# Kernel tuning notes

Measured on AMD Instinct MI355X. Metric: run time of the kernel, lower is better.

Reference implementation:

```python
import jax, jax.numpy as jnp
import numpy as np
from jax import lax

B, N, S, K = 16, 4096, 1024, 32
RADIUS = 0.2
C_IN = 64
BN_EPS = 1e-5


def setup_inputs() -> dict:
    key = jax.random.key(0)
    ks = jax.random.split(key, 6)
    x = jax.random.normal(ks[0], (B, N, 3), dtype=jnp.float32)
    x_complete = jax.random.normal(ks[1], (B, N, C_IN), dtype=jnp.float32)
    W0 = jax.random.normal(ks[2], (64, 67), dtype=jnp.float32) * 0.1
    W1 = jax.random.normal(ks[3], (64, 64), dtype=jnp.float32) * 0.1
    W2 = jax.random.normal(ks[4], (128, 64), dtype=jnp.float32) * 0.1
    return {
        "x": x, "x_complete": x_complete,
        "W0": W0, "b0": jnp.zeros(64), "g0": jnp.ones(64), "be0": jnp.zeros(64),
        "W1": W1, "b1": jnp.zeros(64), "g1": jnp.ones(64), "be1": jnp.zeros(64),
        "W2": W2, "b2": jnp.zeros(128), "g2": jnp.ones(128), "be2": jnp.zeros(128),
    }


def _fps(xyz, n_samples):
    """Farthest point sampling. xyz: [B,N,3] -> indices [B,n_samples] (int32)."""
    b, n, _ = xyz.shape
    batch_ar = jnp.arange(b)

    def step(carry, _):
        dists, farthest = carry                      # [B,N], [B]
        centroid = xyz[batch_ar, farthest]           # [B,3]
        d = jnp.sum((xyz - centroid[:, None, :]) ** 2, axis=-1)  # [B,N]
        dists = jnp.minimum(dists, d)
        nxt = jnp.argmax(dists, axis=-1).astype(jnp.int32)
        return (dists, nxt), farthest

    init = (jnp.full((b, n), 1e10, dtype=xyz.dtype), jnp.zeros(b, dtype=jnp.int32))
    _, idx = lax.scan(step, init, None, length=n_samples)
    return idx.T                                     # [B,n_samples]


def _ball_query(xyz, new_xyz, radius, k):
    """First-k points within radius of each centroid. Returns [B,S,K] int32."""
    b, n, _ = xyz.shape
    # squared distances centroid->point: [B,S,N]
    d2 = jnp.sum((new_xyz[:, :, None, :] - xyz[:, None, :, :]) ** 2, axis=-1)
    idx = jnp.where(d2 <= radius * radius, jnp.arange(n, dtype=jnp.int32), jnp.int32(n))
    idx = jnp.sort(idx, axis=-1)[..., :k]            # first k in index order
    first = idx[..., :1]                             # centroid itself is always in ball
    idx = jnp.where(idx == n, first, idx)
    return jnp.minimum(idx, n - 1)


def _gather_points(pts, idx_flat):
    """pts [B,N,C], idx_flat [B,M] -> [B,M,C]."""
    return jnp.take_along_axis(pts, idx_flat[..., None], axis=1)


def _conv_bn_relu(f, W, b, g, be):
    """f [B,C,M]; 1x1 Conv1d + training-mode BatchNorm1d + ReLU."""
    y = jnp.einsum('bcm,dc->bdm', f, W) + b[None, :, None]
    mu = jnp.mean(y, axis=(0, 2), keepdims=True)
    var = jnp.var(y, axis=(0, 2), keepdims=True)
    y = (y - mu) * lax.rsqrt(var + BN_EPS) * g[None, :, None] + be[None, :, None]
    return jax.nn.relu(y)


def reference(x, x_complete, W0, b0, g0, be0, W1, b1, g1, be1, W2, b2, g2, be2):
    # 1) FPS sampling of S centroids
    fps_idx = _fps(x, S)                                     # [B,S]
    new_xyz = _gather_points(x, fps_idx)                     # [B,S,3]
    # 2) Ball-query grouping of K neighbors per centroid
    idx = _ball_query(x, new_xyz, RADIUS, K)                 # [B,S,K]
    idx_flat = idx.reshape(B, S * K)
    grouped_xyz = _gather_points(x, idx_flat).reshape(B, S, K, 3)
    grouped_xyz = grouped_xyz - new_xyz[:, :, None, :]       # relative coords
    grouped_feat = _gather_points(x_complete, idx_flat).reshape(B, S, K, C_IN)
    f = jnp.concatenate([grouped_xyz, grouped_feat], axis=-1)  # [B,S,K,67]
    # 3) Shared MLP over channel dim (Conv1d k=1 + BN + ReLU), channels-first
    f = f.reshape(B, S * K, 3 + C_IN).transpose(0, 2, 1)     # [B,67,S*K]
    f = _conv_bn_relu(f, W0, b0, g0, be0)
    f = _conv_bn_relu(f, W1, b1, g1, be1)
    f = _conv_bn_relu(f, W2, b2, g2, be2)                    # [B,128,S*K]
    # 4) Max-pool over the K neighbors per centroid
    out = jnp.max(f.reshape(B, 128, S, K), axis=3)           # [B,128,S]
    return out
```

## Files before the change

kernel.cpp:

```cpp
#include <hip/hip_runtime.h>

namespace {
constexpr int kB = 16;
constexpr int kN = 4096;
constexpr int kS = 1024;
constexpr int kK = 32;
constexpr int kCIN = 64;
constexpr int kCF = 67;
constexpr int kFD = 68;
constexpr int kSK = kS * kK;
constexpr int kPT = kB * kSK;
constexpr float kM = 524288.0f;

constexpr size_t kOffIdx   = 196608;
constexpr size_t kOffStats = 2293760;
constexpr size_t kOffScsh  = 2295808;
constexpr size_t kOffU     = 2297856;
constexpr size_t kWsNeedU  = kOffU + (size_t)kB * kN * 64 * sizeof(float);

constexpr int kLdsK = 72;

using bf16x8 = __attribute__((ext_vector_type(8))) short;
using f32x4  = __attribute__((ext_vector_type(4))) float;
}

__device__ __forceinline__ unsigned short f2bf(float f) {
  unsigned u = __float_as_uint(f);
  u += 0x7fffu + ((u >> 16) & 1u);
  return (unsigned short)(u >> 16);
}
__device__ __forceinline__ unsigned pack2bf(float a, float b) {
  return (unsigned)f2bf(a) | ((unsigned)f2bf(b) << 16);
}

__device__ void fps_body(const float* __restrict__ x, float* __restrict__ new_xyz,
                         int b, int tid, char* smem) {
  float* xs = (float*)smem;
  float* ys = xs + kN;
  float* zs = ys + kN;
  float* pv = zs + kN;
  int*   pi = (int*)(pv + 8);
  const int lane = tid & 63;
  const int wid = tid >> 6;
  const float* xb = x + (size_t)b * kN * 3;
  for (int q = tid; q < kN; q += 256) {
    xs[q] = xb[q * 3 + 0];
    ys[q] = xb[q * 3 + 1];
    zs[q] = xb[q * 3 + 2];
  }
  __syncthreads();
  float px[16], py[16], pz[16], dm[16];
#pragma unroll
  for (int j = 0; j < 16; ++j) {
    const int p = tid * 16 + j;
    px[j] = xs[p]; py[j] = ys[p]; pz[j] = zs[p];
    dm[j] = 1e10f;
  }
  int far = 0;
  for (int i = 0; i < kS; ++i) {
    const float cx = xs[far], cy = ys[far], cz = zs[far];
    if (tid == 0) {
      float* o = new_xyz + ((size_t)b * kS + i) * 3;
      o[0] = cx; o[1] = cy; o[2] = cz;
    }
#pragma unroll
    for (int j = 0; j < 16; ++j) {
      const float dx = __fsub_rn(px[j], cx);
      const float dy = __fsub_rn(py[j], cy);
      const float dz = __fsub_rn(pz[j], cz);
      const float t = __fadd_rn(__fadd_rn(__fmul_rn(dx, dx), __fmul_rn(dy, dy)),
                                __fmul_rn(dz, dz));
      dm[j] = fminf(dm[j], t);
    }
    float t8[8], t4[4], t2[2];
#pragma unroll
    for (int j = 0; j < 8; ++j) t8[j] = fmaxf(dm[j], dm[j + 8]);
#pragma unroll
    for (int j = 0; j < 4; ++j) t4[j] = fmaxf(t8[j], t8[j + 4]);
#pragma unroll
    for (int j = 0; j < 2; ++j) t2[j] = fmaxf(t4[j], t4[j + 2]);
    const float bv = fmaxf(t2[0], t2[1]);
    float wv = bv;
#pragma unroll
    for (int k = 1; k < 64; k <<= 1) wv = fmaxf(wv, __shfl_xor(wv, k, 64));
    unsigned msk = 0;
#pragma unroll
    for (int j = 0; j < 16; ++j) msk |= (dm[j] == bv ? 1u : 0u) << j;
    const unsigned long long bal = __ballot(bv == wv);
    const int win = (int)__builtin_ctzll(bal);
    const unsigned wmsk = (unsigned)__shfl((int)msk, win, 64);
    const int wfar = (wid * 64 + win) * 16 + (int)__builtin_ctz(wmsk);
    const int par = i & 1;
    if (lane == 0) { pv[par * 4 + wid] = wv; pi[par * 4 + wid] = wfar; }
    __syncthreads();
    float fv = pv[par * 4 + 0];
    int fi = pi[par * 4 + 0];
#pragma unroll
    for (int w = 1; w < 4; ++w) {
      const float v2 = pv[par * 4 + w];
      const int i2 = pi[par * 4 + w];
      if (v2 > fv) { fv = v2; fi = i2; }
    }
    far = fi;
  }
}

__device__ void u_body(const float* __restrict__ xc, const float* __restrict__ W0,
                       float* __restrict__ U, int ublk, int tid, char* smem) {
  unsigned short* a_lds = (unsigned short*)smem;
  unsigned short* w_lds = (unsigned short*)(smem + 128 * kLdsK * 2);
  const int r0 = ublk * 128;
  {
    const int pt = tid >> 1, half = tid & 1;
    const float4* src = (const float4*)(xc + ((size_t)(r0 + pt)) * 64 + half * 32);
    unsigned* dst = (unsigned*)(a_lds + pt * kLdsK + half * 32);
#pragma unroll
    for (int i = 0; i < 8; ++i) {
      const float4 v = src[i];
      dst[2 * i + 0] = pack2bf(v.x, v.y);
      dst[2 * i + 1] = pack2bf(v.z, v.w);
    }
  }
  for (int e = tid; e < 64 * 64; e += 256) {
    const int d = e >> 6, k2 = e & 63;
    w_lds[d * kLdsK + k2] = f2bf(W0[d * kCF + 3 + k2]);
  }
  __syncthreads();
  const int w = tid >> 6, lane = tid & 63, lr = lane & 15, lk = lane >> 4;
  f32x4 acc[2][4];
#pragma unroll
  for (int mi = 0; mi < 2; ++mi)
#pragma unroll
    for (int ni = 0; ni < 4; ++ni) acc[mi][ni] = (f32x4){0.f, 0.f, 0.f, 0.f};
#pragma unroll
  for (int ks = 0; ks < 2; ++ks) {
    const int k = lk * 8 + ks * 32;
    const bf16x8 a0 = *(const bf16x8*)(a_lds + (32 * w + lr) * kLdsK + k);
    const bf16x8 a1 = *(const bf16x8*)(a_lds + (32 * w + 16 + lr) * kLdsK + k);
#pragma unroll
    for (int ni = 0; ni < 4; ++ni) {
      const bf16x8 bv = *(const bf16x8*)(w_lds + (16 * ni + lr) * kLdsK + k);
      acc[0][ni] = __builtin_amdgcn_mfma_f32_16x16x32_bf16(a0, bv, acc[0][ni], 0, 0, 0);
      acc[1][ni] = __builtin_amdgcn_mfma_f32_16x16x32_bf16(a1, bv, acc[1][ni], 0, 0, 0);
    }
  }
#pragma unroll
  for (int mi = 0; mi < 2; ++mi)
#pragma unroll
    for (int ni = 0; ni < 4; ++ni)
#pragma unroll
      for (int r = 0; r < 4; ++r) {
        const int row = 32 * w + 16 * mi + lk * 4 + r;
        U[((size_t)(r0 + row)) * 64 + 16 * ni + lr] = acc[mi][ni][r];
      }
}

__global__ __launch_bounds__(256) void k1_kernel(const float* __restrict__ x,
                                                 const float* __restrict__ xc,
                                                 const float* __restrict__ W0,
                                                 float* __restrict__ nxyz,
                                                 float* __restrict__ U) {
  __shared__ __align__(16) char smem[49664];
  if (blockIdx.x < 16) fps_body(x, nxyz, blockIdx.x, threadIdx.x, smem);
  else u_body(xc, W0, U, blockIdx.x - 16, threadIdx.x, smem);
}

__global__ __launch_bounds__(256) void ballq_kernel(const float* __restrict__ x,
                                                    const float* __restrict__ new_xyz,
                                                    int* __restrict__ idx) {
  const int g = blockIdx.x * 4 + (threadIdx.x >> 6);
  const int lane = threadIdx.x & 63;
  const int b = g >> 10;
  const float* xb = x + (size_t)b * kN * 3;
  const float nx = new_xyz[g * 3 + 0];
  const float ny = new_xyz[g * 3 + 1];
  const float nz = new_xyz[g * 3 + 2];
  const float RR = (float)(0.2 * 0.2);
  int cnt = 0;
  int first = -1;
  for (int c = 0; c < kN / 64 && cnt < kK; ++c) {
    const int p = c * 64 + lane;
    const float dx = __fsub_rn(xb[p * 3 + 0], nx);
    const float dy = __fsub_rn(xb[p * 3 + 1], ny);
    const float dz = __fsub_rn(xb[p * 3 + 2], nz);
    const float t = __fadd_rn(__fadd_rn(__fmul_rn(dx, dx), __fmul_rn(dy, dy)),
                              __fmul_rn(dz, dz));
    const bool within = (t <= RR);
    const unsigned long long m = __ballot(within);
    if (first < 0 && m != 0ull) first = c * 64 + __builtin_ctzll(m);
    const int pos = cnt + (int)__popcll(m & ((1ull << lane) - 1ull));
    if (within && pos < kK) idx[(size_t)g * kK + pos] = p;
    cnt += (int)__popcll(m);
  }
  for (int k2 = cnt + lane; k2 < kK; k2 += 64) idx[(size_t)g * kK + k2] = first;
}

__global__ __launch_bounds__(256) void stats0_kernel(
    const float* __restrict__ x, const float* __restrict__ nxyz,
    const int* __restrict__ idx, const float* __restrict__ U,
    const float* __restrict__ W0, const float* __restrict__ b0,
    float* __restrict__ stats) {
  __shared__ float4 w0c[64];
  __shared__ float red[128];
  const int tid = threadIdx.x;
  if (tid < 64) w0c[tid] = make_float4(W0[tid * kCF + 0], W0[tid * kCF + 1],
                                       W0[tid * kCF + 2], b0[tid]);
  if (tid < 128) red[tid] = 0.0f;
  __syncthreads();
  const int gid = blockIdx.x * 256 + tid;
  const int half = gid & 1;
  const int pbase = gid >> 1;
  float s[32], q[32];
#pragma unroll
  for (int i = 0; i < 32; ++i) { s[i] = 0.f; q[i] = 0.f; }
  for (int r = 0; r < 8; ++r) {
    const int pt = pbase + r * 65536;
    const int v = idx[pt];
    const int b = pt >> 15;
    const int sc = (pt & (kSK - 1)) >> 5;
    const float* xp = x + ((size_t)b * kN + v) * 3;
    const float* np = nxyz + ((size_t)b * kS + sc) * 3;
    const float rx = xp[0] - np[0], ry = xp[1] - np[1], rz = xp[2] - np[2];
    const float4* up = (const float4*)(U + ((size_t)b * kN + v) * 64 + half * 32);
#pragma unroll
    for (int i = 0; i < 8; ++i) {
      const float4 u4 = up[i];
      const float uu[4] = {u4.x, u4.y, u4.z, u4.w};
#pragma unroll
      for (int j = 0; j < 4; ++j) {
        const float4 wc = w0c[half * 32 + i * 4 + j];
        const float y = uu[j] + rx * wc.x + ry * wc.y + rz * wc.z + wc.w;
        s[i * 4 + j] += y;
        q[i * 4 + j] += y * y;
      }
    }
  }
#pragma unroll
  for (int i = 0; i < 32; ++i) {
    const int c = half * 32 + i;
    atomicAdd(&red[c], s[i]);
    atomicAdd(&red[64 + c], q[i]);
  }
  __syncthreads();
  if (tid < 128) atomicAdd(&stats[tid], red[tid]);
}

template <int STAGE>
__global__ __launch_bounds__(256) void mlp_kernel(
    const float* __restrict__ x, const float* __restrict__ nxyz,
    const int* __restrict__ idx, const float* __restrict__ U,
    const float* __restrict__ W0, const float* __restrict__ b0,
    const float* __restrict__ W1, const float* __restrict__ b1v,
    const float* __restrict__ W2, const float* __restrict__ b2v,
    const float* __restrict__ scsh, float* __restrict__ stats,
    float* __restrict__ out) {
  __shared__ unsigned short a_lds[128 * kLdsK];
  __shared__ unsigned short w_lds[128 * kLdsK];
  __shared__ float red[256];
  __shared__ float4 w0c[64];
  __shared__ float2 sc0l[64];
  const int tid = threadIdx.x;
  const int p0 = blockIdx.x * 128;
  red[tid] = 0.0f;
  if (tid < 64) {
    w0c[tid] = make_float4(W0[tid * kCF + 0], W0[tid * kCF + 1],
                           W0[tid * kCF + 2], b0[tid]);
    sc0l[tid] = make_float2(scsh[tid], scsh[64 + tid]);
  }
  for (int f = tid; f < 64 * 16; f += 256) {
    const int d = f >> 4, k4 = (f & 15) * 4;
    const float4 vw = *(const float4*)(W1 + d * 64 + k4);
    unsigned* dst = (unsigned*)(w_lds + d * kLdsK + k4);
    dst[0] = pack2bf(vw.x, vw.y);
    dst[1] = pack2bf(vw.z, vw.w);
  }
  __syncthreads();

  {
    const int pt = tid >> 1, half = tid & 1;
    const int pg = p0 + pt;
    const int v = idx[pg];
    const int b = pg >> 15;
    const int sct = (pg & (kSK - 1)) >> 5;
    const float* xp = x + ((size_t)b * kN + v) * 3;
    const float* np = nxyz + ((size_t)b * kS + sct) * 3;
    const float rx = xp[0] - np[0], ry = xp[1] - np[1], rz = xp[2] - np[2];
    const float4* up = (const float4*)(U + ((size_t)b * kN + v) * 64 + half * 32);
    unsigned* dst = (unsigned*)(a_lds + pt * kLdsK + half * 32);
#pragma unroll
    for (int i = 0; i < 8; ++i) {
      const float4 u4 = up[i];
      const float uu[4] = {u4.x, u4.y, u4.z, u4.w};
      float a1[4];
#pragma unroll
      for (int j = 0; j < 4; ++j) {
        const int c = half * 32 + i * 4 + j;
        const float4 wc = w0c[c];
        const float y = uu[j] + rx * wc.x + ry * wc.y + rz * wc.z + wc.w;
        const float2 ss = sc0l[c];
        a1[j] = fmaxf(fmaf(y, ss.x, ss.y), 0.0f);
      }
      dst[2 * i + 0] = pack2bf(a1[0], a1[1]);
      dst[2 * i + 1] = pack2bf(a1[2], a1[3]);
    }
  }
  __syncthreads();

  const int w = tid >> 6, lane = tid & 63, lr = lane & 15, lk = lane >> 4;

  f32x4 acc1[2][4];
#pragma unroll
  for (int mi = 0; mi < 2; ++mi)
#pragma unroll
    for (int ni = 0; ni < 4; ++ni) acc1[mi][ni] = (f32x4){0.f, 0.f, 0.f, 0.f};
#pragma unroll
  for (int ks = 0; ks < 2; ++ks) {
    const int k = lk * 8 + ks * 32;
    const bf16x8 a0 = *(const bf16x8*)(a_lds + (32 * w + lr) * kLdsK + k);
    const bf16x8 a1 = *(const bf16x8*)(a_lds + (32 * w + 16 + lr) * kLdsK + k);
#pragma unroll
    for (int ni = 0; ni < 4; ++ni) {
      const bf16x8 bv = *(const bf16x8*)(w_lds + (16 * ni + lr) * kLdsK + k);
      acc1[0][ni] = __builtin_amdgcn_mfma_f32_16x16x32_bf16(a0, bv, acc1[0][ni], 0, 0, 0);
      acc1[1][ni] = __builtin_amdgcn_mfma_f32_16x16x32_bf16(a1, bv, acc1[1][ni], 0, 0, 0);
    }
  }

  if constexpr (STAGE == 1) {
#pragma unroll
    for (int ni = 0; ni < 4; ++ni) {
      const int ch = 16 * ni + lr;
      const float bb = b1v[ch];
      float ss = 0.f, qq = 0.f;
#pragma unroll
      for (int mi = 0; mi < 2; ++mi)
#pragma unroll
        for (int r = 0; r < 4; ++r) {
          const float y = acc1[mi][ni][r] + bb;
          ss += y;
          qq += y * y;
        }
      atomicAdd(&red[ch], ss);
      atomicAdd(&red[64 + ch], qq);
    }
    __syncthreads();
    if (tid < 128) atomicAdd(&stats[128 + tid], red[tid]);
    return;
  } else {
    __syncthreads();
#pragma unroll
    for (int ni = 0; ni < 4; ++ni) {
      const int ch = 16 * ni + lr;
      const float bb = b1v[ch];
      const float sc1 = scsh[128 + ch], sh1 = scsh[192 + ch];
#pragma unroll
      for (int mi = 0; mi < 2; ++mi)
#pragma unroll
        for (int r = 0; r < 4; ++r) {
          const int row = 32 * w + 16 * mi + lk * 4 + r;
          const float val = fmaxf(fmaf(acc1[mi][ni][r] + bb, sc1, sh1), 0.0f);
          a_lds[row * kLdsK + ch] = f2bf(val);
        }
    }
    for (int f = tid; f < 128 * 16; f += 256) {
      const int d = f >> 4, k4 = (f & 15) * 4;
      const float4 vw = *(const float4*)(W2 + d * 64 + k4);
      unsigned* dst = (unsigned*)(w_lds + d * kLdsK + k4);
      dst[0] = pack2bf(vw.x, vw.y);
      dst[1] = pack2bf(vw.z, vw.w);
    }
    __syncthreads();

    f32x4 acc2[2][8];
#pragma unroll
    for (int mi = 0; mi < 2; ++mi)
#pragma unroll
      for (int ni = 0; ni < 8; ++ni) acc2[mi][ni] = (f32x4){0.f, 0.f, 0.f, 0.f};
#pragma unroll
    for (int ks = 0; ks < 2; ++ks) {
      const int k = lk * 8 + ks * 32;
      const bf16x8 a0 = *(const bf16x8*)(a_lds + (32 * w + lr) * kLdsK + k);
      const bf16x8 a1 = *(const bf16x8*)(a_lds + (32 * w + 16 + lr) * kLdsK + k);
#pragma unroll
      for (int ni = 0; ni < 8; ++ni) {
        const bf16x8 bv = *(const bf16x8*)(w_lds + (16 * ni + lr) * kLdsK + k);
        acc2[0][ni] = __builtin_amdgcn_mfma_f32_16x16x32_bf16(a0, bv, acc2[0][ni], 0, 0, 0);
        acc2[1][ni] = __builtin_amdgcn_mfma_f32_16x16x32_bf16(a1, bv, acc2[1][ni], 0, 0, 0);
      }
    }

    if constexpr (STAGE == 2) {
#pragma unroll
      for (int ni = 0; ni < 8; ++ni) {
        const int ch = 16 * ni + lr;
        const float bb = b2v[ch];
        float ss = 0.f, qq = 0.f;
#pragma unroll
        for (int mi = 0; mi < 2; ++mi)
#pragma unroll
          for (int r = 0; r < 4; ++r) {
            const float y = acc2[mi][ni][r] + bb;
            ss += y;
            qq += y * y;
          }
        atomicAdd(&red[ch], ss);
        atomicAdd(&red[128 + ch], qq);
      }
      __syncthreads();
      atomicAdd(&stats[256 + tid], red[tid]);
    } else {
      float mx[8];
#pragma unroll
      for (int ni = 0; ni < 8; ++ni) {
        const int ch = 16 * ni + lr;
        const float bb = b2v[ch];
        const float sc2 = scsh[256 + ch], sh2 = scsh[384 + ch];
        float m = -1.0f;
#pragma unroll
        for (int mi = 0; mi < 2; ++mi)
#pragma unroll
          for (int r = 0; r < 4; ++r)
            m = fmaxf(m, fmaxf(fmaf(acc2[mi][ni][r] + bb, sc2, sh2), 0.0f));
        mx[ni] = m;
      }
#pragma unroll
      for (int ni = 0; ni < 8; ++ni) {
        mx[ni] = fmaxf(mx[ni], __shfl_xor(mx[ni], 16, 64));
        mx[ni] = fmaxf(mx[ni], __shfl_xor(mx[ni], 32, 64));
      }
      const int pg0 = p0 + 32 * w;
      const int ob = pg0 >> 15;
      const int os = (pg0 & (kSK - 1)) >> 5;
      if (lane < 16) {
#pragma unroll
        for (int ni = 0; ni < 8; ++ni)
          out[((size_t)ob * 128 + 16 * ni + lane) * kS + os] = mx[ni];
      }
    }
  }
}

__global__ void finalize_kernel(const float* __restrict__ g, const float* __restrict__ be,
                                const float* __restrict__ st, float* __restrict__ sc,
                                float* __restrict__ sh, int C) {
  const int c = threadIdx.x;
  if (c < C) {
    const float mean = st[c] / kM;
    const float var = st[C + c] / kM - mean * mean;
    const float scale = g[c] / sqrtf(var + 1e-5f);
    sc[c] = scale;
    sh[c] = be[c] - mean * scale;
  }
}

__device__ __forceinline__ void load_bias4(float acc[4][4], const float* b, int tc) {
  const float4 bv = *(const float4*)(b + tc * 4);
  const float bb[4] = {bv.x, bv.y, bv.z, bv.w};
#pragma unroll
  for (int p2 = 0; p2 < 4; ++p2)
#pragma unroll
    for (int ci = 0; ci < 4; ++ci) acc[p2][ci] = bb[ci];
}

__device__ __forceinline__ void gemm4x4(const float* f_lds, const float* w_lds,
                                        int J, int tr, int tc, float acc[4][4]) {
  for (int j = 0; j < J; ++j) {
    const float4 w = *(const float4*)(w_lds + j * 64 + tc * 4);
#pragma unroll
    for (int p2 = 0; p2 < 4; ++p2) {
      const float fv = f_lds[(tr * 4 + p2) * kFD + j];
      acc[p2][0] = fmaf(fv, w.x, acc[p2][0]);
      acc[p2][1] = fmaf(fv, w.y, acc[p2][1]);
      acc[p2][2] = fmaf(fv, w.z, acc[p2][2]);
      acc[p2][3] = fmaf(fv, w.w, acc[p2][3]);
    }
  }
}

__device__ __forceinline__ void bnrelu4(float acc[4][4], const float* scp,
                                        const float* shp, int tc) {
  const float4 s4 = *(const float4*)(scp + tc * 4);
  const float4 h4 = *(const float4*)(shp + tc * 4);
  const float sv[4] = {s4.x, s4.y, s4.z, s4.w};
  const float hv[4] = {h4.x, h4.y, h4.z, h4.w};
#pragma unroll
  for (int p2 = 0; p2 < 4; ++p2)
#pragma unroll
    for (int ci = 0; ci < 4; ++ci)
      acc[p2][ci] = fmaxf(fmaf(acc[p2][ci], sv[ci], hv[ci]), 0.0f);
}

__device__ __forceinline__ void store_a4(const float acc[4][4], float* f_lds,
                                         int tr, int tc) {
#pragma unroll
  for (int p2 = 0; p2 < 4; ++p2)
#pragma unroll
    for (int ci = 0; ci < 4; ++ci)
      f_lds[(tr * 4 + p2) * kFD + tc * 4 + ci] = acc[p2][ci];
}

__device__ __forceinline__ void block_stats4(const float acc[4][4], float* red,
                                             int tc, int C) {
#pragma unroll
  for (int ci = 0; ci < 4; ++ci) {
    const int c = tc * 4 + ci;
    const float sv = acc[0][ci] + acc[1][ci] + acc[2][ci] + acc[3][ci];
    const float qv = acc[0][ci] * acc[0][ci] + acc[1][ci] * acc[1][ci] +
                     acc[2][ci] * acc[2][ci] + acc[3][ci] * acc[3][ci];
    atomicAdd(&red[c], sv);
    atomicAdd(&red[C + c], qv);
  }
}

__device__ __forceinline__ void gather_f(const float* __restrict__ x,
                                         const float* __restrict__ xc,
                                         const float* __restrict__ nxyz,
                                         const int* __restrict__ idx,
                                         float* f_lds, int p0, int tid) {
  const int th_p = tid >> 2;
  const int th_i = tid & 3;
  const int pg = p0 + th_p;
  const int b = pg >> 15;
  const int r = pg & (kSK - 1);
  const int s = r >> 5;
  const int v = idx[pg];
  const float4* feat = (const float4*)(xc + ((size_t)b * kN + v) * kCIN) + th_i * 4;
  const float4 q0 = feat[0], q1 = feat[1], q2 = feat[2], q3 = feat[3];
  float* dst = f_lds + th_p * kFD + 3 + th_i * 16;
  dst[0] = q0.x; dst[1] = q0.y; dst[2] = q0.z; dst[3] = q0.w;
  dst[4] = q1.x; dst[5] = q1.y; dst[6] = q1.z; dst[7] = q1.w;
  dst[8] = q2.x; dst[9] = q2.y; dst[10] = q2.z; dst[11] = q2.w;
  dst[12] = q3.x; dst[13] = q3.y; dst[14] = q3.z; dst[15] = q3.w;
  if (th_i == 0) {
    const float* xp = x + ((size_t)b * kN + v) * 3;
    const float* np = nxyz + ((size_t)b * kS + s) * 3;
    float* fr = f_lds + th_p * kFD;
    fr[0] = __fsub_rn(xp[0], np[0]);
    fr[1] = __fsub_rn(xp[1], np[1]);
    fr[2] = __fsub_rn(xp[2], np[2]);
  }
}

template <int STAGE>
__global__ __launch_bounds__(256) void pass_kernel(
    const float* __restrict__ x, const float* __restrict__ xc,
    const float* __restrict__ W0, const float* __restrict__ b0,
    const float* __restrict__ W1, const float* __restrict__ b1,
    const float* __restrict__ W2, const float* __restrict__ b2,
    const float* __restrict__ nxyz, const int* __restrict__ idx,
    const float* __restrict__ scsh, float* __restrict__ stats,
    float* __restrict__ out) {
  __shared__ float f_lds[64 * kFD];
  __shared__ float w_lds[64 * 128];
  __shared__ float red[256];
  const int tid = threadIdx.x;
  const int p0 = blockIdx.x * 64;
  red[tid] = 0.0f;
  gather_f(x, xc, nxyz, idx, f_lds, p0, tid);
  for (int q = tid; q < 64 * kCF; q += 256) {
    const int c = q / kCF;
    const int j = q - c * kCF;
    w_lds[j * 64 + c] = W0[q];
  }
  __syncthreads();

  const int tc = tid & 15;
  const int tr = tid >> 4;

  float acc[4][4];
  load_bias4(acc, b0, tc);
  gemm4x4(f_lds, w_lds, kCF, tr, tc, acc);

  if constexpr (STAGE == 0) {
    block_stats4(acc, red, tc, 64);
    __syncthreads();
    if (tid < 128) atomicAdd(&stats[tid], red[tid]);
    return;
  } else {
    bnrelu4(acc, scsh + 0, scsh + 64, tc);
    __syncthreads();
    store_a4(acc, f_lds, tr, tc);
    for (int q = tid; q < 64 * 64; q += 256) {
      const int c = q >> 6, j = q & 63;
      w_lds[j * 64 + c] = W1[q];
    }
    __syncthreads();

    load_bias4(acc, b1, tc);
    gemm4x4(f_lds, w_lds, 64, tr, tc, acc);

    if constexpr (STAGE == 1) {
      block_stats4(acc, red, tc, 64);
      __syncthreads();
      if (tid < 128) atomicAdd(&stats[128 + tid], red[tid]);
      return;
    } else {
      bnrelu4(acc, scsh + 128, scsh + 192, tc);
      __syncthreads();
      store_a4(acc, f_lds, tr, tc);
      for (int q = tid; q < 128 * 64; q += 256) {
        const int c = q >> 6, j = q & 63;
        w_lds[j * 128 + c] = W2[q];
      }
      __syncthreads();

      const int c0 = tc * 8;
      float acc2[4][8];
      {
        const float4 ba = *(const float4*)(b2 + c0);
        const float4 bb = *(const float4*)(b2 + c0 + 4);
        const float bv[8] = {ba.x, ba.y, ba.z, ba.w, bb.x, bb.y, bb.z, bb.w};
#pragma unroll
        for (int p2 = 0; p2 < 4; ++p2)
#pragma unroll
          for (int ci = 0; ci < 8; ++ci) acc2[p2][ci] = bv[ci];
      }
      for (int j = 0; j < 64; ++j) {
        const float4 wa = *(const float4*)(w_lds + j * 128 + c0);
        const float4 wb = *(const float4*)(w_lds + j * 128 + c0 + 4);
#pragma unroll
        for (int p2 = 0; p2 < 4; ++p2) {
          const float fv = f_lds[(tr * 4 + p2) * kFD + j];
          acc2[p2][0] = fmaf(fv, wa.x, acc2[p2][0]);
          acc2[p2][1] = fmaf(fv, wa.y, acc2[p2][1]);
          acc2[p2][2] = fmaf(fv, wa.z, acc2[p2][2]);
          acc2[p2][3] = fmaf(fv, wa.w, acc2[p2][3]);
          acc2[p2][4] = fmaf(fv, wb.x, acc2[p2][4]);
          acc2[p2][5] = fmaf(fv, wb.y, acc2[p2][5]);
          acc2[p2][6] = fmaf(fv, wb.z, acc2[p2][6]);
          acc2[p2][7] = fmaf(fv, wb.w, acc2[p2][7]);
        }
      }

      if constexpr (STAGE == 2) {
#pragma unroll
        for (int ci = 0; ci < 8; ++ci) {
          const int c = c0 + ci;
          const float sv = acc2[0][ci] + acc2[1][ci] + acc2[2][ci] + acc2[3][ci];
          const float qv = acc2[0][ci] * acc2[0][ci] + acc2[1][ci] * acc2[1][ci] +
                           acc2[2][ci] * acc2[2][ci] + acc2[3][ci] * acc2[3][ci];
          atomicAdd(&red[c], sv);
          atomicAdd(&red[128 + c], qv);
        }
        __syncthreads();
        atomicAdd(&stats[256 + tid], red[tid]);
        return;
      } else {
        const float4 sa = *(const float4*)(scsh + 256 + c0);
        const float4 sb = *(const float4*)(scsh + 256 + c0 + 4);
        const float4 ha = *(const float4*)(scsh + 384 + c0);
        const float4 hb = *(const float4*)(scsh + 384 + c0 + 4);
        const float scv[8] = {sa.x, sa.y, sa.z, sa.w, sb.x, sb.y, sb.z, sb.w};
        const float shv[8] = {ha.x, ha.y, ha.z, ha.w, hb.x, hb.y, hb.z, hb.w};
        unsigned* redu = (unsigned*)red;
        const int grp = tr >> 3;
#pragma unroll
        for (int ci = 0; ci < 8; ++ci) {
          const float m0 = fmaxf(fmaf(acc2[0][ci], scv[ci], shv[ci]), 0.0f);
          const float m1 = fmaxf(fmaf(acc2[1][ci], scv[ci], shv[ci]), 0.0f);
          const float m2 = fmaxf(fmaf(acc2[2][ci], scv[ci], shv[ci]), 0.0f);
          const float m3 = fmaxf(fmaf(acc2[3][ci], scv[ci], shv[ci]), 0.0f);
          const float mm = fmaxf(fmaxf(m0, m1), fmaxf(m2, m3));
          atomicMax(&redu[grp * 128 + c0 + ci], __float_as_uint(mm));
        }
        __syncthreads();
        const int sg = (p0 >> 5) + (tid >> 7);
        const int ob = sg >> 10;
        const int os = sg & 1023;
        out[((size_t)ob * 128 + (tid & 127)) * kS + os] =
            __uint_as_float(((unsigned*)red)[tid]);
      }
    }
  }
}

extern "C" void kernel_launch(void* const* d_in, const int* in_sizes, int n_in,
                              void* d_out, int out_size, void* d_ws, size_t ws_size,
                              hipStream_t stream) {
  const float* x   = (const float*)d_in[0];
  const float* xc  = (const float*)d_in[1];
  const float* W0  = (const float*)d_in[2];
  const float* b0  = (const float*)d_in[3];
  const float* g0  = (const float*)d_in[4];
  const float* be0 = (const float*)d_in[5];
  const float* W1  = (const float*)d_in[6];
  const float* b1  = (const float*)d_in[7];
  const float* g1  = (const float*)d_in[8];
  const float* be1 = (const float*)d_in[9];
  const float* W2  = (const float*)d_in[10];
  const float* b2  = (const float*)d_in[11];
  const float* g2  = (const float*)d_in[12];
  const float* be2 = (const float*)d_in[13];
  float* out = (float*)d_out;
  char* ws = (char*)d_ws;
  float* nxyz  = (float*)(ws);
  int*   idx   = (int*)(ws + kOffIdx);
  float* stats = (float*)(ws + kOffStats);
  float* scsh  = (float*)(ws + kOffScsh);
  float* U     = (float*)(ws + kOffU);
  (void)in_sizes; (void)n_in; (void)out_size;

  hipMemsetAsync(stats, 0, 512 * sizeof(float), stream);

  if (ws_size >= kWsNeedU) {
    k1_kernel<<<16 + 512, 256, 0, stream>>>(x, xc, W0, nxyz, U);
    ballq_kernel<<<(kB * kS) / 4, 256, 0, stream>>>(x, nxyz, idx);
    stats0_kernel<<<512, 256, 0, stream>>>(x, nxyz, idx, U, W0, b0, stats);
    finalize_kernel<<<1, 128, 0, stream>>>(g0, be0, stats, scsh, scsh + 64, 64);
    mlp_kernel<1><<<kPT / 128, 256, 0, stream>>>(x, nxyz, idx, U, W0, b0, W1, b1,
                                                 W2, b2, scsh, stats, out);
    finalize_kernel<<<1, 128, 0, stream>>>(g1, be1, stats + 128, scsh + 128, scsh + 192, 64);
    mlp_kernel<2><<<kPT / 128, 256, 0, stream>>>(x, nxyz, idx, U, W0, b0, W1, b1,
                                                 W2, b2, scsh, stats, out);
    finalize_kernel<<<1, 128, 0, stream>>>(g2, be2, stats + 256, scsh + 256, scsh + 384, 128);
    mlp_kernel<3><<<kPT / 128, 256, 0, stream>>>(x, nxyz, idx, U, W0, b0, W1, b1,
                                                 W2, b2, scsh, stats, out);
  } else {
    k1_kernel<<<16, 256, 0, stream>>>(x, xc, W0, nxyz, nxyz);
    ballq_kernel<<<(kB * kS) / 4, 256, 0, stream>>>(x, nxyz, idx);
    pass_kernel<0><<<kPT / 64, 256, 0, stream>>>(x, xc, W0, b0, W1, b1, W2, b2,
                                                 nxyz, idx, scsh, stats, out);
    finalize_kernel<<<1, 128, 0, stream>>>(g0, be0, stats, scsh, scsh + 64, 64);
    pass_kernel<1><<<kPT / 64, 256, 0, stream>>>(x, xc, W0, b0, W1, b1, W2, b2,
                                                 nxyz, idx, scsh, stats, out);
    finalize_kernel<<<1, 128, 0, stream>>>(g1, be1, stats + 128, scsh + 128, scsh + 192, 64);
    pass_kernel<2><<<kPT / 64, 256, 0, stream>>>(x, xc, W0, b0, W1, b1, W2, b2,
                                                 nxyz, idx, scsh, stats, out);
    finalize_kernel<<<1, 128, 0, stream>>>(g2, be2, stats + 256, scsh + 256, scsh + 384, 128);
    pass_kernel<3><<<kPT / 64, 256, 0, stream>>>(x, xc, W0, b0, W1, b1, W2, b2,
                                                 nxyz, idx, scsh, stats, out);
  }
}
```

Baseline: 1.314 ms.

## Materialize bf16 layer-1 output, pool pre-BN max/min, use DPP for FPS argmax

The MLP passes are restructured so that layer 1 is computed once and stored to the workspace as bf16. Layer 2 then reads those values instead of recomputing the gather and layer-1 GEMM in both later passes. Layer 2 keeps per-centroid max and min of the pre-BN values, and a small final kernel applies BN plus ReLU, choosing max or min by the sign of the scale, so the third GEMM pass goes away. The FPS argmax reduction swaps shuffles and ballot for DPP row and broadcast reductions and a readlane. The cost is extra workspace traffic for the bf16 intermediate and the pmax/pmin buffers, and the old no-U fallback path is removed.

```diff
diff --git a/kernel.cpp b/kernel.cpp
--- a/kernel.cpp
+++ b/kernel.cpp
@@ -5,9 +5,7 @@
 constexpr int kN = 4096;
 constexpr int kS = 1024;
 constexpr int kK = 32;
-constexpr int kCIN = 64;
 constexpr int kCF = 67;
-constexpr int kFD = 68;
 constexpr int kSK = kS * kK;
 constexpr int kPT = kB * kSK;
 constexpr float kM = 524288.0f;
@@ -17,6 +15,10 @@
 constexpr size_t kOffScsh  = 2295808;
 constexpr size_t kOffU     = 2297856;
 constexpr size_t kWsNeedU  = kOffU + (size_t)kB * kN * 64 * sizeof(float);
+constexpr size_t kOffPmax  = 19075072;
+constexpr size_t kOffPmin  = kOffPmax + 8388608;
+constexpr size_t kOffY1    = kOffPmin + 8388608;
+constexpr size_t kWsNeedF  = kOffY1 + (size_t)kPT * 64 * 2;
 
 constexpr int kLdsK = 72;
 
@@ -31,6 +33,19 @@
 }
 __device__ __forceinline__ unsigned pack2bf(float a, float b) {
   return (unsigned)f2bf(a) | ((unsigned)f2bf(b) << 16);
+}
+
+template <int CTRL, int RM>
+__device__ __forceinline__ float fmax_dpp(float x) {
+  const int m = __builtin_amdgcn_update_dpp(__float_as_int(x), __float_as_int(x),
+                                            CTRL, RM, 0xf, false);
+  return fmaxf(x, __int_as_float(m));
+}
+template <int CTRL, int RM>
+__device__ __forceinline__ unsigned umin_dpp(unsigned x) {
+  const unsigned m = (unsigned)__builtin_amdgcn_update_dpp((int)x, (int)x,
+                                                           CTRL, RM, 0xf, false);
+  return x < m ? x : m;
 }
 
 __device__ void fps_body(const float* __restrict__ x, float* __restrict__ new_xyz,
@@ -72,26 +87,35 @@
                                 __fmul_rn(dz, dz));
       dm[j] = fminf(dm[j], t);
     }
-    float t8[8], t4[4], t2[2];
-#pragma unroll
-    for (int j = 0; j < 8; ++j) t8[j] = fmaxf(dm[j], dm[j + 8]);
-#pragma unroll
-    for (int j = 0; j < 4; ++j) t4[j] = fmaxf(t8[j], t8[j + 4]);
-#pragma unroll
-    for (int j = 0; j < 2; ++j) t2[j] = fmaxf(t4[j], t4[j + 2]);
-    const float bv = fmaxf(t2[0], t2[1]);
-    float wv = bv;
-#pragma unroll
-    for (int k = 1; k < 64; k <<= 1) wv = fmaxf(wv, __shfl_xor(wv, k, 64));
+    const float m0 = fmaxf(fmaxf(dm[0], dm[1]), dm[2]);
+    const float m1 = fmaxf(fmaxf(dm[3], dm[4]), dm[5]);
+    const float m2 = fmaxf(fmaxf(dm[6], dm[7]), dm[8]);
+    const float m3 = fmaxf(fmaxf(dm[9], dm[10]), dm[11]);
+    const float m4 = fmaxf(fmaxf(dm[12], dm[13]), dm[14]);
+    const float n0 = fmaxf(fmaxf(m0, m1), dm[15]);
+    const float n1 = fmaxf(fmaxf(m2, m3), m4);
+    float v = fmaxf(n0, n1);
+    v = fmax_dpp<0x111, 0xf>(v);
+    v = fmax_dpp<0x112, 0xf>(v);
+    v = fmax_dpp<0x114, 0xf>(v);
+    v = fmax_dpp<0x118, 0xf>(v);
+    v = fmax_dpp<0x142, 0xa>(v);
+    v = fmax_dpp<0x143, 0xc>(v);
+    const float wv = __int_as_float(__builtin_amdgcn_readlane(__float_as_int(v), 63));
     unsigned msk = 0;
 #pragma unroll
-    for (int j = 0; j < 16; ++j) msk |= (dm[j] == bv ? 1u : 0u) << j;
-    const unsigned long long bal = __ballot(bv == wv);
-    const int win = (int)__builtin_ctzll(bal);
-    const unsigned wmsk = (unsigned)__shfl((int)msk, win, 64);
-    const int wfar = (wid * 64 + win) * 16 + (int)__builtin_ctz(wmsk);
+    for (int j = 0; j < 16; ++j) msk |= (dm[j] == wv ? 1u : 0u) << j;
+    unsigned cand = msk ? ((unsigned)(tid * 16) + (unsigned)__builtin_ctz(msk))
+                        : 0xffffffffu;
+    cand = umin_dpp<0x111, 0xf>(cand);
+    cand = umin_dpp<0x112, 0xf>(cand);
+    cand = umin_dpp<0x114, 0xf>(cand);
+    cand = umin_dpp<0x118, 0xf>(cand);
+    cand = umin_dpp<0x142, 0xa>(cand);
+    cand = umin_dpp<0x143, 0xc>(cand);
+    const unsigned widx = (unsigned)__builtin_amdgcn_readlane((int)cand, 63);
     const int par = i & 1;
-    if (lane == 0) { pv[par * 4 + wid] = wv; pi[par * 4 + wid] = wfar; }
+    if (lane == 0) { pv[par * 4 + wid] = wv; pi[par * 4 + wid] = (int)widx; }
     __syncthreads();
     float fv = pv[par * 4 + 0];
     int fi = pi[par * 4 + 0];
@@ -245,6 +269,237 @@
   if (tid < 128) atomicAdd(&stats[tid], red[tid]);
 }
 
+__global__ void finalize_kernel(const float* __restrict__ g, const float* __restrict__ be,
+                                const float* __restrict__ st, float* __restrict__ sc,
+                                float* __restrict__ sh, int C) {
+  const int c = threadIdx.x;
+  if (c < C) {
+    const float mean = st[c] / kM;
+    const float var = st[C + c] / kM - mean * mean;
+    const float scale = g[c] / sqrtf(var + 1e-5f);
+    sc[c] = scale;
+    sh[c] = be[c] - mean * scale;
+  }
+}
+
+__global__ __launch_bounds__(256) void mlpA_kernel(
+    const float* __restrict__ x, const float* __restrict__ nxyz,
+    const int* __restrict__ idx, const float* __restrict__ U,
+    const float* __restrict__ W0, const float* __restrict__ b0,
+    const float* __restrict__ W1, const float* __restrict__ b1v,
+    const float* __restrict__ scsh, float* __restrict__ stats,
+    unsigned short* __restrict__ y1out) {
+  __shared__ unsigned short a_lds[128 * kLdsK];
+  __shared__ unsigned short w_lds[64 * kLdsK];
+  __shared__ float red[128];
+  __shared__ float4 w0c[64];
+  __shared__ float2 sc0l[64];
+  const int tid = threadIdx.x;
+  const int p0 = blockIdx.x * 128;
+  if (tid < 128) red[tid] = 0.0f;
+  if (tid < 64) {
+    w0c[tid] = make_float4(W0[tid * kCF + 0], W0[tid * kCF + 1],
+                           W0[tid * kCF + 2], b0[tid]);
+    sc0l[tid] = make_float2(scsh[tid], scsh[64 + tid]);
+  }
+  for (int f = tid; f < 64 * 16; f += 256) {
+    const int d = f >> 4, k4 = (f & 15) * 4;
+    const float4 vw = *(const float4*)(W1 + d * 64 + k4);
+    unsigned* dst = (unsigned*)(w_lds + d * kLdsK + k4);
+    dst[0] = pack2bf(vw.x, vw.y);
+    dst[1] = pack2bf(vw.z, vw.w);
+  }
+  __syncthreads();
+  {
+    const int pt = tid >> 1, half = tid & 1;
+    const int pg = p0 + pt;
+    const int v = idx[pg];
+    const int b = pg >> 15;
+    const int sct = (pg & (kSK - 1)) >> 5;
+    const float* xp = x + ((size_t)b * kN + v) * 3;
+    const float* np = nxyz + ((size_t)b * kS + sct) * 3;
+    const float rx = xp[0] - np[0], ry = xp[1] - np[1], rz = xp[2] - np[2];
+    const float4* up = (const float4*)(U + ((size_t)b * kN + v) * 64 + half * 32);
+    unsigned* dst = (unsigned*)(a_lds + pt * kLdsK + half * 32);
+#pragma unroll
+    for (int i = 0; i < 8; ++i) {
+      const float4 u4 = up[i];
+      const float uu[4] = {u4.x, u4.y, u4.z, u4.w};
+      float a1[4];
+#pragma unroll
+      for (int j = 0; j < 4; ++j) {
+        const int c = half * 32 + i * 4 + j;
+        const float4 wc = w0c[c];
+        const float y = uu[j] + rx * wc.x + ry * wc.y + rz * wc.z + wc.w;
+        const float2 ss = sc0l[c];
+        a1[j] = fmaxf(fmaf(y, ss.x, ss.y), 0.0f);
+      }
+      dst[2 * i + 0] = pack2bf(a1[0], a1[1]);
+      dst[2 * i + 1] = pack2bf(a1[2], a1[3]);
+    }
+  }
+  __syncthreads();
+
+  const int w = tid >> 6, lane = tid & 63, lr = lane & 15, lk = lane >> 4;
+  f32x4 acc1[2][4];
+#pragma unroll
+  for (int mi = 0; mi < 2; ++mi)
+#pragma unroll
+    for (int ni = 0; ni < 4; ++ni) acc1[mi][ni] = (f32x4){0.f, 0.f, 0.f, 0.f};
+#pragma unroll
+  for (int ks = 0; ks < 2; ++ks) {
+    const int k = lk * 8 + ks * 32;
+    const bf16x8 a0 = *(const bf16x8*)(a_lds + (32 * w + lr) * kLdsK + k);
+    const bf16x8 a1 = *(const bf16x8*)(a_lds + (32 * w + 16 + lr) * kLdsK + k);
+#pragma unroll
+    for (int ni = 0; ni < 4; ++ni) {
+      const bf16x8 bv = *(const bf16x8*)(w_lds + (16 * ni + lr) * kLdsK + k);
+      acc1[0][ni] = __builtin_amdgcn_mfma_f32_16x16x32_bf16(a0, bv, acc1[0][ni], 0, 0, 0);
+      acc1[1][ni] = __builtin_amdgcn_mfma_f32_16x16x32_bf16(a1, bv, acc1[1][ni], 0, 0, 0);
+    }
+  }
+#pragma unroll
+  for (int ni = 0; ni < 4; ++ni) {
+    const int ch = 16 * ni + lr;
+    const float bb = b1v[ch];
+    float ss = 0.f, qq = 0.f;
+#pragma unroll
+    for (int mi = 0; mi < 2; ++mi)
+#pragma unroll
+      for (int r = 0; r < 4; ++r) {
+        const float y = acc1[mi][ni][r] + bb;
+        ss += y;
+        qq += y * y;
+        const int row = 32 * w + 16 * mi + lk * 4 + r;
+        a_lds[row * kLdsK + ch] = f2bf(y);
+      }
+    atomicAdd(&red[ch], ss);
+    atomicAdd(&red[64 + ch], qq);
+  }
+  __syncthreads();
+  {
+    const int row = tid >> 1, hf = tid & 1;
+    const uint4* s4 = (const uint4*)(a_lds + row * kLdsK + hf * 32);
+    uint4* d4 = (uint4*)(y1out + (size_t)(p0 + row) * 64 + hf * 32);
+    d4[0] = s4[0]; d4[1] = s4[1]; d4[2] = s4[2]; d4[3] = s4[3];
+  }
+  if (tid < 128) atomicAdd(&stats[128 + tid], red[tid]);
+}
+
+__global__ __launch_bounds__(256) void mlpB_kernel(
+    const unsigned short* __restrict__ y1in, const float* __restrict__ W2,
+    const float* __restrict__ b2v, const float* __restrict__ scsh,
+    float* __restrict__ stats, float* __restrict__ pmax,
+    float* __restrict__ pmin) {
+  __shared__ unsigned short a_lds[128 * kLdsK];
+  __shared__ unsigned short w_lds[128 * kLdsK];
+  __shared__ float red[256];
+  __shared__ float2 s1l[64];
+  const int tid = threadIdx.x;
+  const int p0 = blockIdx.x * 128;
+  red[tid] = 0.0f;
+  if (tid < 64) s1l[tid] = make_float2(scsh[128 + tid], scsh[192 + tid]);
+  __syncthreads();
+  for (int f = tid; f < 128 * 16; f += 256) {
+    const int d = f >> 4, k4 = (f & 15) * 4;
+    const float4 vw = *(const float4*)(W2 + d * 64 + k4);
+    unsigned* dst = (unsigned*)(w_lds + d * kLdsK + k4);
+    dst[0] = pack2bf(vw.x, vw.y);
+    dst[1] = pack2bf(vw.z, vw.w);
+  }
+  {
+    const int row = tid >> 1, hf = tid & 1;
+    const uint4* src = (const uint4*)(y1in + (size_t)(p0 + row) * 64 + hf * 32);
+    const uint4 qa = src[0], qb = src[1], qc = src[2], qd = src[3];
+    const unsigned in[16] = {qa.x, qa.y, qa.z, qa.w, qb.x, qb.y, qb.z, qb.w,
+                             qc.x, qc.y, qc.z, qc.w, qd.x, qd.y, qd.z, qd.w};
+    unsigned* dst = (unsigned*)(a_lds + row * kLdsK) + hf * 16;
+#pragma unroll
+    for (int i2 = 0; i2 < 16; ++i2) {
+      const unsigned u = in[i2];
+      const int ch0 = hf * 32 + i2 * 2;
+      const float2 sA = s1l[ch0];
+      const float2 sB = s1l[ch0 + 1];
+      const float flo = __uint_as_float(u << 16);
+      const float fhi = __uint_as_float(u & 0xffff0000u);
+      const float alo = fmaxf(fmaf(flo, sA.x, sA.y), 0.0f);
+      const float ahi = fmaxf(fmaf(fhi, sB.x, sB.y), 0.0f);
+      dst[i2] = pack2bf(alo, ahi);
+    }
+  }
+  __syncthreads();
+
+  const int w = tid >> 6, lane = tid & 63, lr = lane & 15, lk = lane >> 4;
+  f32x4 acc2[2][8];
+#pragma unroll
+  for (int mi = 0; mi < 2; ++mi)
+#pragma unroll
+    for (int ni = 0; ni < 8; ++ni) acc2[mi][ni] = (f32x4){0.f, 0.f, 0.f, 0.f};
+#pragma unroll
+  for (int ks = 0; ks < 2; ++ks) {
+    const int k = lk * 8 + ks * 32;
+    const bf16x8 a0 = *(const bf16x8*)(a_lds + (32 * w + lr) * kLdsK + k);
+    const bf16x8 a1 = *(const bf16x8*)(a_lds + (32 * w + 16 + lr) * kLdsK + k);
+#pragma unroll
+    for (int ni = 0; ni < 8; ++ni) {
+      const bf16x8 bv = *(const bf16x8*)(w_lds + (16 * ni + lr) * kLdsK + k);
+      acc2[0][ni] = __builtin_amdgcn_mfma_f32_16x16x32_bf16(a0, bv, acc2[0][ni], 0, 0, 0);
+      acc2[1][ni] = __builtin_amdgcn_mfma_f32_16x16x32_bf16(a1, bv, acc2[1][ni], 0, 0, 0);
+    }
+  }
+  float mxv[8], mnv[8];
+#pragma unroll
+  for (int ni = 0; ni < 8; ++ni) {
+    const int ch = 16 * ni + lr;
+    const float bb = b2v[ch];
+    float ss = 0.f, qq = 0.f;
+    float mx = -3.4e38f, mn = 3.4e38f;
+#pragma unroll
+    for (int mi = 0; mi < 2; ++mi)
+#pragma unroll
+      for (int r = 0; r < 4; ++r) {
+        const float a = acc2[mi][ni][r];
+        const float y = a + bb;
+        ss += y;
+        qq += y * y;
+        mx = fmaxf(mx, a);
+        mn = fminf(mn, a);
+      }
+    atomicAdd(&red[ch], ss);
+    atomicAdd(&red[128 + ch], qq);
+    mx = fmaxf(mx, __shfl_xor(mx, 16, 64));
+    mx = fmaxf(mx, __shfl_xor(mx, 32, 64));
+    mn = fminf(mn, __shfl_xor(mn, 16, 64));
+    mn = fminf(mn, __shfl_xor(mn, 32, 64));
+    mxv[ni] = mx + bb;
+    mnv[ni] = mn + bb;
+  }
+  __syncthreads();
+  atomicAdd(&stats[256 + tid], red[tid]);
+  const int pg0 = p0 + 32 * w;
+  const int ob = pg0 >> 15;
+  const int os = (pg0 & (kSK - 1)) >> 5;
+  if (lane < 16) {
+#pragma unroll
+    for (int ni = 0; ni < 8; ++ni) {
+      const size_t off = ((size_t)ob * 128 + 16 * ni + lane) * kS + os;
+      pmax[off] = mxv[ni];
+      pmin[off] = mnv[ni];
+    }
+  }
+}
+
+__global__ __launch_bounds__(256) void poolbn_kernel(
+    const float* __restrict__ pmax, const float* __restrict__ pmin,
+    const float* __restrict__ scsh, float* __restrict__ out) {
+  const int gid = blockIdx.x * 256 + threadIdx.x;
+  const int c = (gid >> 10) & 127;
+  const float sc = scsh[256 + c];
+  const float sh = scsh[384 + c];
+  const float p = (sc >= 0.f) ? pmax[gid] : pmin[gid];
+  out[gid] = fmaxf(fmaf(p, sc, sh), 0.0f);
+}
+
 template <int STAGE>
 __global__ __launch_bounds__(256) void mlp_kernel(
     const float* __restrict__ x, const float* __restrict__ nxyz,
@@ -275,7 +530,6 @@
     dst[1] = pack2bf(vw.z, vw.w);
   }
   __syncthreads();
-
   {
     const int pt = tid >> 1, half = tid & 1;
     const int pg = p0 + pt;
@@ -307,7 +561,6 @@
   __syncthreads();
 
   const int w = tid >> 6, lane = tid & 63, lr = lane & 15, lk = lane >> 4;
-
   f32x4 acc1[2][4];
 #pragma unroll
   for (int mi = 0; mi < 2; ++mi)
@@ -435,240 +688,6 @@
 #pragma unroll
         for (int ni = 0; ni < 8; ++ni)
           out[((size_t)ob * 128 + 16 * ni + lane) * kS + os] = mx[ni];
-      }
-    }
-  }
-}
-
-__global__ void finalize_kernel(const float* __restrict__ g, const float* __restrict__ be,
-                                const float* __restrict__ st, float* __restrict__ sc,
-                                float* __restrict__ sh, int C) {
-  const int c = threadIdx.x;
-  if (c < C) {
-    const float mean = st[c] / kM;
-    const float var = st[C + c] / kM - mean * mean;
-    const float scale = g[c] / sqrtf(var + 1e-5f);
-    sc[c] = scale;
-    sh[c] = be[c] - mean * scale;
-  }
-}
-
-__device__ __forceinline__ void load_bias4(float acc[4][4], const float* b, int tc) {
-  const float4 bv = *(const float4*)(b + tc * 4);
-  const float bb[4] = {bv.x, bv.y, bv.z, bv.w};
-#pragma unroll
-  for (int p2 = 0; p2 < 4; ++p2)
-#pragma unroll
-    for (int ci = 0; ci < 4; ++ci) acc[p2][ci] = bb[ci];
-}
-
-__device__ __forceinline__ void gemm4x4(const float* f_lds, const float* w_lds,
-                                        int J, int tr, int tc, float acc[4][4]) {
-  for (int j = 0; j < J; ++j) {
-    const float4 w = *(const float4*)(w_lds + j * 64 + tc * 4);
-#pragma unroll
-    for (int p2 = 0; p2 < 4; ++p2) {
-      const float fv = f_lds[(tr * 4 + p2) * kFD + j];
-      acc[p2][0] = fmaf(fv, w.x, acc[p2][0]);
-      acc[p2][1] = fmaf(fv, w.y, acc[p2][1]);
-      acc[p2][2] = fmaf(fv, w.z, acc[p2][2]);
-      acc[p2][3] = fmaf(fv, w.w, acc[p2][3]);
-    }
-  }
-}
-
-__device__ __forceinline__ void bnrelu4(float acc[4][4], const float* scp,
-                                        const float* shp, int tc) {
-  const float4 s4 = *(const float4*)(scp + tc * 4);
-  const float4 h4 = *(const float4*)(shp + tc * 4);
-  const float sv[4] = {s4.x, s4.y, s4.z, s4.w};
-  const float hv[4] = {h4.x, h4.y, h4.z, h4.w};
-#pragma unroll
-  for (int p2 = 0; p2 < 4; ++p2)
-#pragma unroll
-    for (int ci = 0; ci < 4; ++ci)
-      acc[p2][ci] = fmaxf(fmaf(acc[p2][ci], sv[ci], hv[ci]), 0.0f);
-}
-
-__device__ __forceinline__ void store_a4(const float acc[4][4], float* f_lds,
-                                         int tr, int tc) {
-#pragma unroll
-  for (int p2 = 0; p2 < 4; ++p2)
-#pragma unroll
-    for (int ci = 0; ci < 4; ++ci)
-      f_lds[(tr * 4 + p2) * kFD + tc * 4 + ci] = acc[p2][ci];
-}
-
-__device__ __forceinline__ void block_stats4(const float acc[4][4], float* red,
-                                             int tc, int C) {
-#pragma unroll
-  for (int ci = 0; ci < 4; ++ci) {
-    const int c = tc * 4 + ci;
-    const float sv = acc[0][ci] + acc[1][ci] + acc[2][ci] + acc[3][ci];
-    const float qv = acc[0][ci] * acc[0][ci] + acc[1][ci] * acc[1][ci] +
-                     acc[2][ci] * acc[2][ci] + acc[3][ci] * acc[3][ci];
-    atomicAdd(&red[c], sv);
-    atomicAdd(&red[C + c], qv);
-  }
-}
-
-__device__ __forceinline__ void gather_f(const float* __restrict__ x,
-                                         const float* __restrict__ xc,
-                                         const float* __restrict__ nxyz,
-                                         const int* __restrict__ idx,
-                                         float* f_lds, int p0, int tid) {
-  const int th_p = tid >> 2;
-  const int th_i = tid & 3;
-  const int pg = p0 + th_p;
-  const int b = pg >> 15;
-  const int r = pg & (kSK - 1);
-  const int s = r >> 5;
-  const int v = idx[pg];
-  const float4* feat = (const float4*)(xc + ((size_t)b * kN + v) * kCIN) + th_i * 4;
-  const float4 q0 = feat[0], q1 = feat[1], q2 = feat[2], q3 = feat[3];
-  float* dst = f_lds + th_p * kFD + 3 + th_i * 16;
-  dst[0] = q0.x; dst[1] = q0.y; dst[2] = q0.z; dst[3] = q0.w;
-  dst[4] = q1.x; dst[5] = q1.y; dst[6] = q1.z; dst[7] = q1.w;
-  dst[8] = q2.x; dst[9] = q2.y; dst[10] = q2.z; dst[11] = q2.w;
-  dst[12] = q3.x; dst[13] = q3.y; dst[14] = q3.z; dst[15] = q3.w;
-  if (th_i == 0) {
-    const float* xp = x + ((size_t)b * kN + v) * 3;
-    const float* np = nxyz + ((size_t)b * kS + s) * 3;
-    float* fr = f_lds + th_p * kFD;
-    fr[0] = __fsub_rn(xp[0], np[0]);
-    fr[1] = __fsub_rn(xp[1], np[1]);
-    fr[2] = __fsub_rn(xp[2], np[2]);
-  }
-}
-
-template <int STAGE>
-__global__ __launch_bounds__(256) void pass_kernel(
-    const float* __restrict__ x, const float* __restrict__ xc,
-    const float* __restrict__ W0, const float* __restrict__ b0,
-    const float* __restrict__ W1, const float* __restrict__ b1,
-    const float* __restrict__ W2, const float* __restrict__ b2,
-    const float* __restrict__ nxyz, const int* __restrict__ idx,
-    const float* __restrict__ scsh, float* __restrict__ stats,
-    float* __restrict__ out) {
-  __shared__ float f_lds[64 * kFD];
-  __shared__ float w_lds[64 * 128];
-  __shared__ float red[256];
-  const int tid = threadIdx.x;
-  const int p0 = blockIdx.x * 64;
-  red[tid] = 0.0f;
-  gather_f(x, xc, nxyz, idx, f_lds, p0, tid);
-  for (int q = tid; q < 64 * kCF; q += 256) {
-    const int c = q / kCF;
-    const int j = q - c * kCF;
-    w_lds[j * 64 + c] = W0[q];
-  }
-  __syncthreads();
-
-  const int tc = tid & 15;
-  const int tr = tid >> 4;
-
-  float acc[4][4];
-  load_bias4(acc, b0, tc);
-  gemm4x4(f_lds, w_lds, kCF, tr, tc, acc);
-
-  if constexpr (STAGE == 0) {
-    block_stats4(acc, red, tc, 64);
-    __syncthreads();
-    if (tid < 128) atomicAdd(&stats[tid], red[tid]);
-    return;
-  } else {
-    bnrelu4(acc, scsh + 0, scsh + 64, tc);
-    __syncthreads();
-    store_a4(acc, f_lds, tr, tc);
-    for (int q = tid; q < 64 * 64; q += 256) {
-      const int c = q >> 6, j = q & 63;
-      w_lds[j * 64 + c] = W1[q];
-    }
-    __syncthreads();
-
-    load_bias4(acc, b1, tc);
-    gemm4x4(f_lds, w_lds, 64, tr, tc, acc);
-
-    if constexpr (STAGE == 1) {
-      block_stats4(acc, red, tc, 64);
-      __syncthreads();
-      if (tid < 128) atomicAdd(&stats[128 + tid], red[tid]);
-      return;
-    } else {
-      bnrelu4(acc, scsh + 128, scsh + 192, tc);
-      __syncthreads();
-      store_a4(acc, f_lds, tr, tc);
-      for (int q = tid; q < 128 * 64; q += 256) {
-        const int c = q >> 6, j = q & 63;
-        w_lds[j * 128 + c] = W2[q];
-      }
-      __syncthreads();
-
-      const int c0 = tc * 8;
-      float acc2[4][8];
-      {
-        const float4 ba = *(const float4*)(b2 + c0);
-        const float4 bb = *(const float4*)(b2 + c0 + 4);
-        const float bv[8] = {ba.x, ba.y, ba.z, ba.w, bb.x, bb.y, bb.z, bb.w};
-#pragma unroll
-        for (int p2 = 0; p2 < 4; ++p2)
-#pragma unroll
-          for (int ci = 0; ci < 8; ++ci) acc2[p2][ci] = bv[ci];
-      }
-      for (int j = 0; j < 64; ++j) {
-        const float4 wa = *(const float4*)(w_lds + j * 128 + c0);
-        const float4 wb = *(const float4*)(w_lds + j * 128 + c0 + 4);
-#pragma unroll
-        for (int p2 = 0; p2 < 4; ++p2) {
-          const float fv = f_lds[(tr * 4 + p2) * kFD + j];
-          acc2[p2][0] = fmaf(fv, wa.x, acc2[p2][0]);
-          acc2[p2][1] = fmaf(fv, wa.y, acc2[p2][1]);
-          acc2[p2][2] = fmaf(fv, wa.z, acc2[p2][2]);
-          acc2[p2][3] = fmaf(fv, wa.w, acc2[p2][3]);
-          acc2[p2][4] = fmaf(fv, wb.x, acc2[p2][4]);
-          acc2[p2][5] = fmaf(fv, wb.y, acc2[p2][5]);
-          acc2[p2][6] = fmaf(fv, wb.z, acc2[p2][6]);
-          acc2[p2][7] = fmaf(fv, wb.w, acc2[p2][7]);
-        }
-      }
-
-      if constexpr (STAGE == 2) {
-#pragma unroll
-        for (int ci = 0; ci < 8; ++ci) {
-          const int c = c0 + ci;
-          const float sv = acc2[0][ci] + acc2[1][ci] + acc2[2][ci] + acc2[3][ci];
-          const float qv = acc2[0][ci] * acc2[0][ci] + acc2[1][ci] * acc2[1][ci] +
-                           acc2[2][ci] * acc2[2][ci] + acc2[3][ci] * acc2[3][ci];
-          atomicAdd(&red[c], sv);
-          atomicAdd(&red[128 + c], qv);
-        }
-        __syncthreads();
-        atomicAdd(&stats[256 + tid], red[tid]);
-        return;
-      } else {
-        const float4 sa = *(const float4*)(scsh + 256 + c0);
-        const float4 sb = *(const float4*)(scsh + 256 + c0 + 4);
-        const float4 ha = *(const float4*)(scsh + 384 + c0);
-        const float4 hb = *(const float4*)(scsh + 384 + c0 + 4);
-        const float scv[8] = {sa.x, sa.y, sa.z, sa.w, sb.x, sb.y, sb.z, sb.w};
-        const float shv[8] = {ha.x, ha.y, ha.z, ha.w, hb.x, hb.y, hb.z, hb.w};
-        unsigned* redu = (unsigned*)red;
-        const int grp = tr >> 3;
-#pragma unroll
-        for (int ci = 0; ci < 8; ++ci) {
-          const float m0 = fmaxf(fmaf(acc2[0][ci], scv[ci], shv[ci]), 0.0f);
-          const float m1 = fmaxf(fmaf(acc2[1][ci], scv[ci], shv[ci]), 0.0f);
-          const float m2 = fmaxf(fmaf(acc2[2][ci], scv[ci], shv[ci]), 0.0f);
-          const float m3 = fmaxf(fmaf(acc2[3][ci], scv[ci], shv[ci]), 0.0f);
-          const float mm = fmaxf(fmaxf(m0, m1), fmaxf(m2, m3));
-          atomicMax(&redu[grp * 128 + c0 + ci], __float_as_uint(mm));
-        }
-        __syncthreads();
-        const int sg = (p0 >> 5) + (tid >> 7);
-        const int ob = sg >> 10;
-        const int os = sg & 1023;
-        out[((size_t)ob * 128 + (tid & 127)) * kS + os] =
-            __uint_as_float(((unsigned*)red)[tid]);
       }
     }
   }
@@ -698,15 +717,25 @@
   float* stats = (float*)(ws + kOffStats);
   float* scsh  = (float*)(ws + kOffScsh);
   float* U     = (float*)(ws + kOffU);
+  float* pmax  = (float*)(ws + kOffPmax);
+  float* pmin  = (float*)(ws + kOffPmin);
+  unsigned short* y1 = (unsigned short*)(ws + kOffY1);
   (void)in_sizes; (void)n_in; (void)out_size;
 
   hipMemsetAsync(stats, 0, 512 * sizeof(float), stream);
-
-  if (ws_size >= kWsNeedU) {
-    k1_kernel<<<16 + 512, 256, 0, stream>>>(x, xc, W0, nxyz, U);
-    ballq_kernel<<<(kB * kS) / 4, 256, 0, stream>>>(x, nxyz, idx);
-    stats0_kernel<<<512, 256, 0, stream>>>(x, nxyz, idx, U, W0, b0, stats);
-    finalize_kernel<<<1, 128, 0, stream>>>(g0, be0, stats, scsh, scsh + 64, 64);
+  k1_kernel<<<16 + 512, 256, 0, stream>>>(x, xc, W0, nxyz, U);
+  ballq_kernel<<<(kB * kS) / 4, 256, 0, stream>>>(x, nxyz, idx);
+  stats0_kernel<<<512, 256, 0, stream>>>(x, nxyz, idx, U, W0, b0, stats);
+  finalize_kernel<<<1, 128, 0, stream>>>(g0, be0, stats, scsh, scsh + 64, 64);
+
+  if (ws_size >= kWsNeedF) {
+    mlpA_kernel<<<kPT / 128, 256, 0, stream>>>(x, nxyz, idx, U, W0, b0, W1, b1,
+                                               scsh, stats, y1);
+    finalize_kernel<<<1, 128, 0, stream>>>(g1, be1, stats + 128, scsh + 128, scsh + 192, 64);
+    mlpB_kernel<<<kPT / 128, 256, 0, stream>>>(y1, W2, b2, scsh, stats, pmax, pmin);
+    finalize_kernel<<<1, 128, 0, stream>>>(g2, be2, stats + 256, scsh + 256, scsh + 384, 128);
+    poolbn_kernel<<<(kB * 128 * kS) / 256, 256, 0, stream>>>(pmax, pmin, scsh, out);
+  } else {
     mlp_kernel<1><<<kPT / 128, 256, 0, stream>>>(x, nxyz, idx, U, W0, b0, W1, b1,
                                                  W2, b2, scsh, stats, out);
     finalize_kernel<<<1, 128, 0, stream>>>(g1, be1, stats + 128, scsh + 128, scsh + 192, 64);
@@ -715,19 +744,5 @@
     finalize_kernel<<<1, 128, 0, stream>>>(g2, be2, stats + 256, scsh + 256, scsh + 384, 128);
     mlp_kernel<3><<<kPT / 128, 256, 0, stream>>>(x, nxyz, idx, U, W0, b0, W1, b1,
                                                  W2, b2, scsh, stats, out);
-  } else {
-    k1_kernel<<<16, 256, 0, stream>>>(x, xc, W0, nxyz, nxyz);
-    ballq_kernel<<<(kB * kS) / 4, 256, 0, stream>>>(x, nxyz, idx);
-    pass_kernel<0><<<kPT / 64, 256, 0, stream>>>(x, xc, W0, b0, W1, b1, W2, b2,
-                                                 nxyz, idx, scsh, stats, out);
-    finalize_kernel<<<1, 128, 0, stream>>>(g0, be0, stats, scsh, scsh + 64, 64);
-    pass_kernel<1><<<kPT / 64, 256, 0, stream>>>(x, xc, W0, b0, W1, b1, W2, b2,
-                                                 nxyz, idx, scsh, stats, out);
-    finalize_kernel<<<1, 128, 0, stream>>>(g1, be1, stats + 128, scsh + 128, scsh + 192, 64);
-    pass_kernel<2><<<kPT / 64, 256, 0, stream>>>(x, xc, W0, b0, W1, b1, W2, b2,
-                                                 nxyz, idx, scsh, stats, out);
-    finalize_kernel<<<1, 128, 0, stream>>>(g2, be2, stats + 256, scsh + 256, scsh + 384, 128);
-    pass_kernel<3><<<kPT / 64, 256, 0, stream>>>(x, xc, W0, b0, W1, b1, W2, b2,
-                                                 nxyz, idx, scsh, stats, out);
-  }
-}
+  }
+}
```

Measured after the change: 1.187 ms. 9.6% less time.
